# Performance work log

Hardware: AMD Instinct MI355X
Metric: run time of the kernel (lower is better)

Reference implementation:

```python
import jax, jax.numpy as jnp
import numpy as np
import math

L, D, H, PK, N = 3, 512, 8, 8, 3072
DK = D // H


def _layernorm(x, s, b):
    m = jnp.mean(x, axis=-1, keepdims=True)
    v = jnp.mean((x - m) ** 2, axis=-1, keepdims=True)
    return (x - m) / jnp.sqrt(v + 1e-6) * s + b


def setup_inputs() -> dict:
    key = jax.random.key(0)
    ks = jax.random.split(key, 12)
    p = lambda k, shape: jax.random.normal(k, shape, jnp.float32) * (1.0 / math.sqrt(shape[-1]))
    x = jax.random.normal(ks[0], (N, D), jnp.float32)
    adm = jax.random.randint(ks[1], (N, N), 0, PK, jnp.int32)
    return {
        "x": x,
        "adm": adm,
        "ln_att_s": jnp.ones((L, D), jnp.float32),
        "ln_att_b": jnp.zeros((L, D), jnp.float32),
        "Wq": p(ks[2], (L, D, D)),
        "Wk": p(ks[3], (L, D, D)),
        "Wv": p(ks[4], (L, D, D)),
        "rel_k": p(ks[5], (L, PK, DK)),
        "Wg": p(ks[6], (L, D, D)) * 0.0,  # gating weight init to 0 in original
        "bg": jnp.ones((L, D), jnp.float32),  # gating bias init to 1
        "Wo": p(ks[7], (L, D, D)),
        "bo": jnp.zeros((L, D), jnp.float32),
        "ln_ff_s": jnp.ones((L, D), jnp.float32),
        "ln_ff_b": jnp.zeros((L, D), jnp.float32),
        "W1": p(ks[8], (L, D, 2 * D)),
        "b1": jnp.zeros((L, 2 * D), jnp.float32),
        "W2": p(ks[9], (L, 2 * D, D)),
        "b2": jnp.zeros((L, D), jnp.float32),
    }


def reference(x, adm, ln_att_s, ln_att_b, Wq, Wk, Wv, rel_k, Wg, bg, Wo, bo,
              ln_ff_s, ln_ff_b, W1, b1, W2, b2):
    att_scores = []
    idx = jnp.broadcast_to(adm[None], (H, N, N))  # one_hot(gpm) @ r  ==  gather r along PK
    for n in range(L):
        xn = _layernorm(x, ln_att_s[n], ln_att_b[n])  # same layer_norm applied to x_q and x_k
        q = (xn @ Wq[n]).reshape(N, H, DK).transpose(1, 0, 2)  # [H,N,DK]
        k = (xn @ Wk[n]).reshape(N, H, DK).transpose(1, 0, 2)
        v = (xn @ Wv[n]).reshape(N, H, DK).transpose(1, 0, 2)
        attn1 = jnp.einsum('hid,hjd->hij', q, k)  # [H,N,N]
        rq = jnp.einsum('hid,pd->hip', q, rel_k[n])  # [H,N,PK]
        attn2 = jnp.take_along_axis(rq, idx, axis=2)  # [H,N,N]
        attn = jax.nn.softmax((attn1 + attn2) / math.sqrt(DK), axis=-1)
        out = jnp.einsum('hij,hjd->hid', attn, v).transpose(1, 0, 2).reshape(N, D)
        gate = jax.nn.sigmoid(xn @ Wg[n] + bg[n])
        m = (out * gate) @ Wo[n] + bo[n]
        # FFN with pre-layernorm, residual: x = x + pff(x + m)
        y = x + m
        yn = _layernorm(y, ln_ff_s[n], ln_ff_b[n])
        ff = jax.nn.gelu(yn @ W1[n] + b1[n], approximate=True) @ W2[n] + b2[n]
        x = x + ff
        att_scores.append(attn)
    return (x, jnp.stack(att_scores))
```

## Files before the change

kernel.cpp:

```cpp
#include <hip/hip_runtime.h>
#include <math.h>

#define NT 3072
#define DIM 512
#define NH 8
#define DKH 64
#define PKN 8
#define D2 1024
#define NL 3
#define QS 2048

typedef float4 f4;
typedef unsigned short ushort_t;
typedef unsigned char uchar_t;
typedef __attribute__((ext_vector_type(8))) short s8x;
typedef __attribute__((ext_vector_type(4))) float fx4;

#define MFMA(a, b, c) __builtin_amdgcn_mfma_f32_16x16x32_bf16(a, b, c, 0, 0, 0)
#define EX2(x) __builtin_amdgcn_exp2f(x)

__device__ __forceinline__ float b2f(ushort_t u) {
  union { unsigned int x; float f; } c;
  c.x = (unsigned int)u << 16;
  return c.f;
}
__device__ __forceinline__ ushort_t f2b(float f) {
  union { float f; unsigned int x; } c;
  c.f = f;
  unsigned int r = (c.x + 0x7FFFu + ((c.x >> 16) & 1u)) >> 16;
  return (ushort_t)r;
}
__device__ __forceinline__ float wred_sum(float v) {
#pragma unroll
  for (int off = 32; off > 0; off >>= 1) v += __shfl_xor(v, off);
  return v;
}
__device__ __forceinline__ void gload16(const ushort_t* g, ushort_t* l) {
  __builtin_amdgcn_global_load_lds(
      (const __attribute__((address_space(1))) unsigned int*)(const void*)g,
      (__attribute__((address_space(3))) unsigned int*)(void*)l, 16, 0, 0);
}

__global__ __launch_bounds__(256) void ln_bf16_kernel(
    const float* __restrict__ x, const float* __restrict__ s,
    const float* __restrict__ b, ushort_t* __restrict__ out) {
  int row = blockIdx.x;
  const float* xr = x + (size_t)row * DIM;
  int t = threadIdx.x;
  float v0 = xr[t], v1 = xr[t + 256];
  float sum = wred_sum(v0 + v1);
  float sq = wred_sum(v0 * v0 + v1 * v1);
  __shared__ float ss[4], s2[4];
  if ((t & 63) == 0) { ss[t >> 6] = sum; s2[t >> 6] = sq; }
  __syncthreads();
  float tot = ss[0] + ss[1] + ss[2] + ss[3];
  float tot2 = s2[0] + s2[1] + s2[2] + s2[3];
  float mean = tot * (1.0f / DIM);
  float var = tot2 * (1.0f / DIM) - mean * mean;
  float inv = rsqrtf(var + 1e-6f);
  ushort_t* orow = out + (size_t)row * DIM;
  orow[t] = f2b((v0 - mean) * inv * s[t] + b[t]);
  orow[t + 256] = f2b((v1 - mean) * inv * s[t + 256] + b[t + 256]);
}

__device__ __forceinline__ void tconv_body(const float* __restrict__ W,
                                           ushort_t* __restrict__ Wt, int K,
                                           int Nc, int tx, int ty) {
  __shared__ float Ls[64][65];
  int t = threadIdx.x;
  int n0 = tx * 64, k0 = ty * 64;
  int rr = t >> 4, cc = (t & 15) * 4;
#pragma unroll
  for (int p = 0; p < 4; ++p) {
    f4 v = *(const f4*)&W[(size_t)(k0 + rr + p * 16) * Nc + n0 + cc];
    Ls[rr + p * 16][cc + 0] = v.x;
    Ls[rr + p * 16][cc + 1] = v.y;
    Ls[rr + p * 16][cc + 2] = v.z;
    Ls[rr + p * 16][cc + 3] = v.w;
  }
  __syncthreads();
  int nr = t >> 2, kc = (t & 3) * 16;
  ushort_t tmp[16];
#pragma unroll
  for (int e = 0; e < 16; ++e) tmp[e] = f2b(Ls[kc + e][nr]);
  ushort_t* dst = &Wt[(size_t)(n0 + nr) * K + k0 + kc];
  *(uint4*)dst = *(uint4*)&tmp[0];
  *(uint4*)(dst + 8) = *(uint4*)&tmp[8];
}

__global__ __launch_bounds__(256) void wprep_kernel(
    const float* __restrict__ Wq, const float* __restrict__ Wk,
    const float* __restrict__ Wv, const float* __restrict__ Wg,
    const float* __restrict__ Wo, const float* __restrict__ W1,
    const float* __restrict__ W2, ushort_t* __restrict__ Wt) {
  int bid = blockIdx.x;
  if (bid < 320) {
    int job = bid >> 6, tile = bid & 63;
    const float* src = job == 0 ? Wq : job == 1 ? Wk : job == 2 ? Wv
                       : job == 3 ? Wg : Wo;
    tconv_body(src, Wt + (size_t)job * 262144, 512, 512, tile & 7, tile >> 3);
  } else if (bid < 448) {
    int tile = bid - 320;
    tconv_body(W1, Wt + 1310720, 512, 1024, tile & 15, tile >> 4);
  } else {
    int tile = bid - 448;
    tconv_body(W2, Wt + 1835008, 1024, 512, tile & 7, tile >> 3);
  }
}

__global__ __launch_bounds__(256) void adm8_kernel(const int* __restrict__ adm,
                                                   uchar_t* __restrict__ out) {
  size_t i = ((size_t)blockIdx.x * 256 + threadIdx.x) * 4;
  int4 v = *(const int4*)&adm[i];
  unsigned int b = (unsigned)(v.x & 255) | ((unsigned)(v.y & 255) << 8) |
                   ((unsigned)(v.z & 255) << 16) | ((unsigned)(v.w & 255) << 24);
  *(unsigned int*)&out[i] = b;
}

__global__ __launch_bounds__(256) void vt_kernel(const ushort_t* __restrict__ v,
                                                 ushort_t* __restrict__ vbT) {
  int jt = blockIdx.x, h = blockIdx.y;
  __shared__ ushort_t L[64][72];
  int t = threadIdx.x;
  int r = t >> 2, c = (t & 3) * 16;
  const ushort_t* src = v + (size_t)(jt * 64 + r) * QS + h * 64 + c;
  *(uint4*)&L[r][c] = *(const uint4*)src;
  *(uint4*)&L[r][c + 8] = *(const uint4*)(src + 8);
  __syncthreads();
  int d = t >> 2, j0 = (t & 3) * 16;
  ushort_t tmp[16];
#pragma unroll
  for (int e = 0; e < 16; ++e) tmp[e] = L[j0 + e][d];
  ushort_t* dst = vbT + (size_t)(h * 64 + d) * NT + jt * 64 + j0;
  *(uint4*)dst = *(uint4*)&tmp[0];
  *(uint4*)(dst + 8) = *(uint4*)&tmp[8];
}

template <int ACT, bool OBF>
__global__ __launch_bounds__(256) void gemm64(
    const ushort_t* __restrict__ A, const ushort_t* __restrict__ Bt,
    const float* __restrict__ bias, const float* __restrict__ res,
    void* __restrict__ Cp, int K, int ldc, float scale) {
  __shared__ __align__(16) ushort_t As[2][4096];
  __shared__ __align__(16) ushort_t Bs[2][4096];
  int t = threadIdx.x;
  int i0 = blockIdx.y * 64, j0 = blockIdx.x * 64;
  int w = t >> 6, l = t & 63;
  int wm = w >> 1, wn = w & 1;
  int lr = l >> 4, lc = l & 15;
  int sr = t >> 3;
  int sc8 = ((t & 7) ^ (sr & 7)) * 8;
  const ushort_t* aS = A + (size_t)(i0 + sr) * K + sc8;
  const ushort_t* bS = Bt + (size_t)(j0 + sr) * K + sc8;
  int sA0 = (wm * 32 + lc) * 64 + ((lr ^ (lc & 7)) * 8);
  int sA1 = (wm * 32 + 16 + lc) * 64 + ((lr ^ (lc & 7)) * 8);
  int sB0 = (wn * 32 + lc) * 64 + ((lr ^ (lc & 7)) * 8);
  int sB1 = (wn * 32 + 16 + lc) * 64 + ((lr ^ (lc & 7)) * 8);

  fx4 acc[2][2] = {};

#define G64_STAGE(buf, k0)                                                   \
  {                                                                          \
    gload16(aS + (k0), &As[buf][t * 8]);                                     \
    gload16(aS + (k0) + (size_t)32 * K, &As[buf][2048 + t * 8]);             \
    gload16(bS + (k0), &Bs[buf][t * 8]);                                     \
    gload16(bS + (k0) + (size_t)32 * K, &Bs[buf][2048 + t * 8]);             \
  }

  G64_STAGE(0, 0);
  __syncthreads();
  int cur = 0;
  for (int k0 = 0; k0 < K; k0 += 64) {
    if (k0 + 64 < K) G64_STAGE(cur ^ 1, k0 + 64);
    const ushort_t* Ac = As[cur];
    const ushort_t* Bc = Bs[cur];
#pragma unroll
    for (int ks = 0; ks < 2; ++ks) {
      s8x a0 = *(const s8x*)&Ac[sA0 ^ (ks << 5)];
      s8x a1 = *(const s8x*)&Ac[sA1 ^ (ks << 5)];
      s8x b0 = *(const s8x*)&Bc[sB0 ^ (ks << 5)];
      s8x b1 = *(const s8x*)&Bc[sB1 ^ (ks << 5)];
      acc[0][0] = MFMA(a0, b0, acc[0][0]);
      acc[0][1] = MFMA(a0, b1, acc[0][1]);
      acc[1][0] = MFMA(a1, b0, acc[1][0]);
      acc[1][1] = MFMA(a1, b1, acc[1][1]);
    }
    __syncthreads();
    cur ^= 1;
  }
#undef G64_STAGE

#pragma unroll
  for (int ms = 0; ms < 2; ++ms) {
#pragma unroll
    for (int ns = 0; ns < 2; ++ns) {
#pragma unroll
      for (int r = 0; r < 4; ++r) {
        int i = i0 + wm * 32 + ms * 16 + lr * 4 + r;
        int j = j0 + wn * 32 + ns * 16 + lc;
        float o = acc[ms][ns][r] * scale;
        if (ACT == 3) {
          if (blockIdx.x < 8) o *= 0.18033688011112042f;
          if (blockIdx.x >= 24) {
            o += bias[j & 511];
            o = 1.0f / (1.0f + __expf(-o));
          }
        } else {
          if (bias) o += bias[j];
          if (ACT == 1) {
            o = 1.0f / (1.0f + __expf(-o));
          } else if (ACT == 2) {
            float xx = o;
            float c2 = 1.5957691216057308f * (xx + 0.044715f * xx * xx * xx);
            o = xx / (1.0f + __expf(-c2));
          }
          if (res) o += res[(size_t)i * ldc + j];
        }
        if (OBF)
          ((ushort_t*)Cp)[(size_t)i * ldc + j] = f2b(o);
        else
          ((float*)Cp)[(size_t)i * ldc + j] = o;
      }
    }
  }
}

__device__ __forceinline__ float rq_sel(const unsigned int* rqt,
                                        unsigned int idx) {
  unsigned int d01 = (idx & 2) ? rqt[1] : rqt[0];
  unsigned int d23 = (idx & 2) ? rqt[3] : rqt[2];
  unsigned int dd = (idx & 4) ? d23 : d01;
  unsigned int r = (idx & 1) ? (dd & 0xffff0000u) : (dd << 16);
  return __uint_as_float(r);
}

__global__ __launch_bounds__(256) void attn_kernel(
    const ushort_t* __restrict__ xqkvg, const ushort_t* __restrict__ vbT,
    const float* __restrict__ relk, const uchar_t* __restrict__ adm8,
    float* __restrict__ att, ushort_t* __restrict__ av) {
  int f = blockIdx.y * (NT / 32) + blockIdx.x;
  int h = f & 7;
  int i0 = (f >> 3) * 32;
  int t = threadIdx.x, w = t >> 6, l = t & 63;
  int lr = l >> 4, lc = l & 15;
  int ig = w & 1, jh = w >> 1;
  int i_loc = ig * 16 + lc;
  int i = i0 + i_loc;

  __shared__ __align__(16) ushort_t Kd[2][2][4096];
  __shared__ __align__(16) ushort_t Vd[2][2][4096];
  __shared__ __align__(16) ushort_t Ps[2][2048];
  __shared__ float MLs[2][2][16][2];

  int stgo = ig * 2048;
  int srow = ig * 32 + (l >> 3);
  int kp8 = ((l & 7) ^ ((l >> 3) & 7)) * 8;
  const ushort_t* kSrc0 =
      xqkvg + 512 + (size_t)(jh * 64 + srow) * QS + h * 64 + kp8;
  const ushort_t* vSrc0 = vbT + (size_t)(h * 64 + srow) * NT + jh * 64 + kp8;
  const uchar_t* admp0 = adm8 + (size_t)i * NT + jh * 64 + lr * 4;

#define STAGE_K(buf, tt)                                                     \
  {                                                                          \
    const ushort_t* ks_ = kSrc0 + (size_t)(tt) * 128 * QS;                   \
    gload16(ks_, Kd[buf][jh] + stgo);                                        \
    gload16(ks_ + (size_t)8 * QS, Kd[buf][jh] + stgo + 512);                 \
    gload16(ks_ + (size_t)16 * QS, Kd[buf][jh] + stgo + 1024);               \
    gload16(ks_ + (size_t)24 * QS, Kd[buf][jh] + stgo + 1536);               \
  }
#define STAGE_V(buf, tt)                                                     \
  {                                                                          \
    const ushort_t* vs_ = vSrc0 + (tt) * 128;                                \
    gload16(vs_, Vd[buf][jh] + stgo);                                        \
    gload16(vs_ + (size_t)8 * NT, Vd[buf][jh] + stgo + 512);                 \
    gload16(vs_ + (size_t)16 * NT, Vd[buf][jh] + stgo + 1024);               \
    gload16(vs_ + (size_t)24 * NT, Vd[buf][jh] + stgo + 1536);               \
  }

  STAGE_K(0, 0);

  const ushort_t* qp = xqkvg + (size_t)i * QS + h * 64 + lr * 8;
  s8x qf0 = *(const s8x*)qp;
  s8x qf1 = *(const s8x*)(qp + 32);

  unsigned int rqt[4];
  {
    const ushort_t* q0 = (const ushort_t*)&qf0;
    const ushort_t* q1 = (const ushort_t*)&qf1;
    float sp[8];
#pragma unroll
    for (int p = 0; p < 8; ++p) {
      const float* rp = relk + p * 64 + lr * 8;
      float s = 0.f;
#pragma unroll
      for (int e = 0; e < 8; ++e) s = fmaf(b2f(q0[e]), rp[e], s);
#pragma unroll
      for (int e = 0; e < 8; ++e) s = fmaf(b2f(q1[e]), rp[32 + e], s);
      s += __shfl_xor(s, 16);
      s += __shfl_xor(s, 32);
      sp[p] = s;
    }
#pragma unroll
    for (int j = 0; j < 4; ++j)
      rqt[j] = (unsigned int)f2b(sp[2 * j]) |
               ((unsigned int)f2b(sp[2 * j + 1]) << 16);
  }

  int sw = (lc & 7);
  int a_b0 = lc * 64 + ((lr ^ sw) << 3);
  int a_b1 = lc * 64 + (((4 + lr) ^ sw) << 3);
  int pb0 = i_loc * 64 + ((lr ^ sw) << 3);
  int pb1 = i_loc * 64 + (((4 + lr) ^ sw) << 3);
  int swz8 = sw << 3;

  float m_run = -1e30f, l_run = 0.f;
  __syncthreads();

  {
    int cur = 0;
    for (int tt = 0; tt < 24; ++tt) {
      if (tt < 23) STAGE_K(cur ^ 1, tt + 1);
      const ushort_t* KS = Kd[cur][jh];
      const uchar_t* admp = admp0 + tt * 128;
      fx4 sacc[4] = {};
#pragma unroll
      for (int ja = 0; ja < 4; ++ja) {
        s8x a0 = *(const s8x*)(KS + a_b0 + ja * 1024);
        s8x a1 = *(const s8x*)(KS + a_b1 + ja * 1024);
        sacc[ja] = MFMA(a0, qf0, sacc[ja]);
        sacc[ja] = MFMA(a1, qf1, sacc[ja]);
      }
      float sv[4][4];
      float tm = -1e30f;
#pragma unroll
      for (int ja = 0; ja < 4; ++ja) {
        unsigned int aw = *(const unsigned int*)(admp + ja * 16);
#pragma unroll
        for (int r = 0; r < 4; ++r) {
          float vv = sacc[ja][r] + rq_sel(rqt, (aw >> (8 * r)) & 7u);
          sv[ja][r] = vv;
          tm = fmaxf(tm, vv);
        }
      }
      float mn = fmaxf(m_run, tm);
      float sum = 0.f;
#pragma unroll
      for (int ja = 0; ja < 4; ++ja)
#pragma unroll
        for (int r = 0; r < 4; ++r) sum += EX2(sv[ja][r] - mn);
      l_run = l_run * EX2(m_run - mn) + sum;
      m_run = mn;
      __syncthreads();
      cur ^= 1;
    }
  }

  STAGE_K(0, 0);
  STAGE_V(0, 0);

#pragma unroll
  for (int off = 16; off <= 32; off <<= 1) {
    float mo = __shfl_xor(m_run, off), lo = __shfl_xor(l_run, off);
    float mn = fmaxf(m_run, mo);
    l_run = l_run * EX2(m_run - mn) + lo * EX2(mo - mn);
    m_run = mn;
  }
  if (l < 16) {
    MLs[jh][ig][lc][0] = m_run;
    MLs[jh][ig][lc][1] = l_run;
  }
  __syncthreads();
  {
    float mo = MLs[jh ^ 1][ig][lc][0], lo = MLs[jh ^ 1][ig][lc][1];
    float mn = fmaxf(m_run, mo);
    l_run = l_run * EX2(m_run - mn) + lo * EX2(mo - mn);
    m_run = mn;
  }
  float lofs = m_run + __log2f(l_run);

  fx4 oacc[4] = {};
  float* attb = att + ((size_t)h * NT + i0) * NT;
  ushort_t* PS = Ps[jh];
  int jh64 = jh * 64;
  {
    int cur = 0;
    for (int tt = 0; tt < 24; ++tt) {
      if (tt < 23) {
        STAGE_K(cur ^ 1, tt + 1);
        STAGE_V(cur ^ 1, tt + 1);
      }
      const ushort_t* KS = Kd[cur][jh];
      const ushort_t* VS = Vd[cur][jh];
      const uchar_t* admp = admp0 + tt * 128;
      fx4 sacc[4] = {};
#pragma unroll
      for (int ja = 0; ja < 4; ++ja) {
        s8x a0 = *(const s8x*)(KS + a_b0 + ja * 1024);
        s8x a1 = *(const s8x*)(KS + a_b1 + ja * 1024);
        sacc[ja] = MFMA(a0, qf0, sacc[ja]);
        sacc[ja] = MFMA(a1, qf1, sacc[ja]);
      }
#pragma unroll
      for (int ja = 0; ja < 4; ++ja) {
        unsigned int aw = *(const unsigned int*)(admp + ja * 16);
        float p0 = EX2(sacc[ja][0] + rq_sel(rqt, aw & 7u) - lofs);
        float p1 = EX2(sacc[ja][1] + rq_sel(rqt, (aw >> 8) & 7u) - lofs);
        float p2 = EX2(sacc[ja][2] + rq_sel(rqt, (aw >> 16) & 7u) - lofs);
        float p3 = EX2(sacc[ja][3] + rq_sel(rqt, (aw >> 24) & 7u) - lofs);
        unsigned int w01 = (unsigned int)f2b(p0) | ((unsigned int)f2b(p1) << 16);
        unsigned int w23 = (unsigned int)f2b(p2) | ((unsigned int)f2b(p3) << 16);
        int cb = ja * 16 + lr * 4;
        *(unsigned int*)&PS[i_loc * 64 + (cb ^ swz8)] = w01;
        *(unsigned int*)&PS[i_loc * 64 + ((cb + 2) ^ swz8)] = w23;
      }
      {
        int uu = ig * 64 + l;
        int row = uu >> 2, cs = (uu & 3) * 16;
        int rsw = (row & 7) << 3;
        uint4 A_ = *(const uint4*)&PS[row * 64 + (cs ^ rsw)];
        uint4 B_ = *(const uint4*)&PS[row * 64 + ((cs + 8) ^ rsw)];
        const ushort_t* ap = (const ushort_t*)&A_;
        const ushort_t* bp = (const ushort_t*)&B_;
        float* op = attb + (size_t)row * NT + tt * 128 + jh64 + cs;
        f4 o0 = {b2f(ap[0]), b2f(ap[1]), b2f(ap[2]), b2f(ap[3])};
        f4 o1 = {b2f(ap[4]), b2f(ap[5]), b2f(ap[6]), b2f(ap[7])};
        f4 o2 = {b2f(bp[0]), b2f(bp[1]), b2f(bp[2]), b2f(bp[3])};
        f4 o3 = {b2f(bp[4]), b2f(bp[5]), b2f(bp[6]), b2f(bp[7])};
        *(f4*)(op + 0) = o0;
        *(f4*)(op + 4) = o1;
        *(f4*)(op + 8) = o2;
        *(f4*)(op + 12) = o3;
      }
#pragma unroll
      for (int ks = 0; ks < 2; ++ks) {
        s8x pf = *(const s8x*)(PS + (ks == 0 ? pb0 : pb1));
#pragma unroll
        for (int nd = 0; nd < 4; ++nd) {
          s8x vf = *(const s8x*)(VS + (ks == 0 ? a_b0 : a_b1) + nd * 1024);
          oacc[nd] = MFMA(vf, pf, oacc[nd]);
        }
      }
      __syncthreads();
      cur ^= 1;
    }
  }
#undef STAGE_K
#undef STAGE_V

  ushort_t* PsF = &Ps[0][0];
  int swzO = (i_loc & 7) << 3;
  if (jh == 1) {
#pragma unroll
    for (int nd = 0; nd < 4; ++nd) {
      int d0 = nd * 16 + lr * 4;
      unsigned int lo = (unsigned int)f2b(oacc[nd][0]) |
                        ((unsigned int)f2b(oacc[nd][1]) << 16);
      unsigned int hi = (unsigned int)f2b(oacc[nd][2]) |
                        ((unsigned int)f2b(oacc[nd][3]) << 16);
      uint2 pk = {lo, hi};
      *(uint2*)&PsF[i_loc * 64 + (d0 ^ swzO)] = pk;
    }
  }
  __syncthreads();
  if (jh == 0) {
    const ushort_t* gp = xqkvg + (size_t)i * QS + 1536 + h * 64;
#pragma unroll
    for (int nd = 0; nd < 4; ++nd) {
      int d0 = nd * 16 + lr * 4;
      uint2 pk = *(const uint2*)&PsF[i_loc * 64 + (d0 ^ swzO)];
      const ushort_t* pp = (const ushort_t*)&pk;
      uint2 gk = *(const uint2*)(gp + d0);
      const ushort_t* gg = (const ushort_t*)&gk;
      ushort_t ot[4];
#pragma unroll
      for (int r = 0; r < 4; ++r)
        ot[r] = f2b((oacc[nd][r] + b2f(pp[r])) * b2f(gg[r]));
      *(uint2*)&av[(size_t)i * DIM + h * 64 + d0] = *(uint2*)ot;
    }
  }
}

extern "C" void kernel_launch(void* const* d_in, const int* in_sizes, int n_in,
                              void* d_out, int out_size, void* d_ws,
                              size_t ws_size, hipStream_t stream) {
  const float* x_in = (const float*)d_in[0];
  const int* adm = (const int*)d_in[1];
  const float* ln_att_s = (const float*)d_in[2];
  const float* ln_att_b = (const float*)d_in[3];
  const float* Wq = (const float*)d_in[4];
  const float* Wk = (const float*)d_in[5];
  const float* Wv = (const float*)d_in[6];
  const float* rel_k = (const float*)d_in[7];
  const float* Wg = (const float*)d_in[8];
  const float* bg = (const float*)d_in[9];
  const float* Wo = (const float*)d_in[10];
  const float* bo = (const float*)d_in[11];
  const float* ln_ff_s = (const float*)d_in[12];
  const float* ln_ff_b = (const float*)d_in[13];
  const float* W1 = (const float*)d_in[14];
  const float* b1 = (const float*)d_in[15];
  const float* W2 = (const float*)d_in[16];
  const float* b2 = (const float*)d_in[17];
  float* out = (float*)d_out;

  const size_t ND = (size_t)NT * DIM;
  char* ws = (char*)d_ws;
  float* x_cur = (float*)ws;
  float* y = (float*)(ws + 6291456);
  ushort_t* xqkvg = (ushort_t*)(ws + 12582912);
  ushort_t* avb = (ushort_t*)(ws + 25165824);
  ushort_t* xnb = (ushort_t*)(ws + 28311552);
  ushort_t* vbT = (ushort_t*)(ws + 31457280);
  uchar_t* adm8 = (uchar_t*)(ws + 34603008);
  ushort_t* Wt = (ushort_t*)(ws + 44040192);
  ushort_t* h1b = xqkvg;

  hipMemcpyAsync(x_cur, x_in, ND * sizeof(float), hipMemcpyDeviceToDevice,
                 stream);
  adm8_kernel<<<(NT * NT) / 1024, 256, 0, stream>>>(adm, adm8);

  dim3 gQKVG(32, NT / 64);
  dim3 gA(8, NT / 64);
  dim3 gF1(16, NT / 64);

  for (int n = 0; n < NL; ++n) {
    float* att = out + ND + (size_t)n * NH * NT * NT;
    size_t wo = (size_t)n * DIM * DIM;

    wprep_kernel<<<576, 256, 0, stream>>>(Wq + wo, Wk + wo, Wv + wo, Wg + wo,
                                          Wo + wo, W1 + (size_t)n * DIM * D2,
                                          W2 + (size_t)n * D2 * DIM, Wt);
    ln_bf16_kernel<<<NT, 256, 0, stream>>>(x_cur, ln_att_s + n * DIM,
                                           ln_att_b + n * DIM, xnb);
    gemm64<3, true><<<gQKVG, 256, 0, stream>>>(xnb, Wt, bg + n * DIM, nullptr,
                                               xqkvg, DIM, QS, 1.0f);
    vt_kernel<<<dim3(NT / 64, NH), 256, 0, stream>>>(xqkvg + 1024, vbT);
    attn_kernel<<<dim3(NT / 32, NH), 256, 0, stream>>>(
        xqkvg, vbT, rel_k + n * PKN * DKH, adm8, att, avb);
    gemm64<0, false><<<gA, 256, 0, stream>>>(avb, Wt + 1048576, bo + n * DIM,
                                             x_cur, y, DIM, DIM, 1.0f);
    ln_bf16_kernel<<<NT, 256, 0, stream>>>(y, ln_ff_s + n * DIM,
                                           ln_ff_b + n * DIM, xnb);
    gemm64<2, true><<<gF1, 256, 0, stream>>>(xnb, Wt + 1310720, b1 + n * D2,
                                             nullptr, h1b, DIM, D2, 1.0f);
    gemm64<0, false><<<gA, 256, 0, stream>>>(h1b, Wt + 1835008, b2 + n * DIM,
                                             x_cur, x_cur, D2, DIM, 1.0f);
  }
  hipMemcpyAsync(out, x_cur, ND * sizeof(float), hipMemcpyDeviceToDevice,
                 stream);
}
```

Before: 1.057 ms.

## Batch weight prep, drop residual copies, use nontemporal attention stores

Weight transpose/convert for all three layers now runs in one launch indexed by blockIdx.y, instead of one launch per layer. The initial and final device-to-device copies of x are removed: layer 0 reads x_in directly and the last FFN GEMM writes straight into the output. Attention-probability writes to the large score tensor become nontemporal stores, which keeps them from polluting cache. A __syncthreads is inserted before the P tile is read back from shared memory, which looks like a race fix but adds one barrier per iteration.

```diff
diff --git a/kernel.cpp b/kernel.cpp
--- a/kernel.cpp
+++ b/kernel.cpp
@@ -93,18 +93,23 @@
     const float* __restrict__ Wv, const float* __restrict__ Wg,
     const float* __restrict__ Wo, const float* __restrict__ W1,
     const float* __restrict__ W2, ushort_t* __restrict__ Wt) {
+  int n = blockIdx.y;
+  size_t wo5 = (size_t)n * 262144;
+  ushort_t* Wtl = Wt + (size_t)n * 2359296;
   int bid = blockIdx.x;
   if (bid < 320) {
     int job = bid >> 6, tile = bid & 63;
-    const float* src = job == 0 ? Wq : job == 1 ? Wk : job == 2 ? Wv
-                       : job == 3 ? Wg : Wo;
-    tconv_body(src, Wt + (size_t)job * 262144, 512, 512, tile & 7, tile >> 3);
+    const float* src = job == 0 ? Wq + wo5 : job == 1 ? Wk + wo5
+                       : job == 2 ? Wv + wo5 : job == 3 ? Wg + wo5 : Wo + wo5;
+    tconv_body(src, Wtl + (size_t)job * 262144, 512, 512, tile & 7, tile >> 3);
   } else if (bid < 448) {
     int tile = bid - 320;
-    tconv_body(W1, Wt + 1310720, 512, 1024, tile & 15, tile >> 4);
+    tconv_body(W1 + (size_t)n * 524288, Wtl + 1310720, 512, 1024, tile & 15,
+               tile >> 4);
   } else {
     int tile = bid - 448;
-    tconv_body(W2, Wt + 1835008, 1024, 512, tile & 7, tile >> 3);
+    tconv_body(W2 + (size_t)n * 524288, Wtl + 1835008, 1024, 512, tile & 7,
+               tile >> 3);
   }
 }
 
@@ -413,6 +418,7 @@
         *(unsigned int*)&PS[i_loc * 64 + (cb ^ swz8)] = w01;
         *(unsigned int*)&PS[i_loc * 64 + ((cb + 2) ^ swz8)] = w23;
       }
+      __syncthreads();
       {
         int uu = ig * 64 + l;
         int row = uu >> 2, cs = (uu & 3) * 16;
@@ -422,14 +428,14 @@
         const ushort_t* ap = (const ushort_t*)&A_;
         const ushort_t* bp = (const ushort_t*)&B_;
         float* op = attb + (size_t)row * NT + tt * 128 + jh64 + cs;
-        f4 o0 = {b2f(ap[0]), b2f(ap[1]), b2f(ap[2]), b2f(ap[3])};
-        f4 o1 = {b2f(ap[4]), b2f(ap[5]), b2f(ap[6]), b2f(ap[7])};
-        f4 o2 = {b2f(bp[0]), b2f(bp[1]), b2f(bp[2]), b2f(bp[3])};
-        f4 o3 = {b2f(bp[4]), b2f(bp[5]), b2f(bp[6]), b2f(bp[7])};
-        *(f4*)(op + 0) = o0;
-        *(f4*)(op + 4) = o1;
-        *(f4*)(op + 8) = o2;
-        *(f4*)(op + 12) = o3;
+        fx4 o0 = {b2f(ap[0]), b2f(ap[1]), b2f(ap[2]), b2f(ap[3])};
+        fx4 o1 = {b2f(ap[4]), b2f(ap[5]), b2f(ap[6]), b2f(ap[7])};
+        fx4 o2 = {b2f(bp[0]), b2f(bp[1]), b2f(bp[2]), b2f(bp[3])};
+        fx4 o3 = {b2f(bp[4]), b2f(bp[5]), b2f(bp[6]), b2f(bp[7])};
+        __builtin_nontemporal_store(o0, (fx4*)(op + 0));
+        __builtin_nontemporal_store(o1, (fx4*)(op + 4));
+        __builtin_nontemporal_store(o2, (fx4*)(op + 8));
+        __builtin_nontemporal_store(o3, (fx4*)(op + 12));
       }
 #pragma unroll
       for (int ks = 0; ks < 2; ++ks) {
@@ -515,9 +521,9 @@
   ushort_t* Wt = (ushort_t*)(ws + 44040192);
   ushort_t* h1b = xqkvg;
 
-  hipMemcpyAsync(x_cur, x_in, ND * sizeof(float), hipMemcpyDeviceToDevice,
-                 stream);
   adm8_kernel<<<(NT * NT) / 1024, 256, 0, stream>>>(adm, adm8);
+  wprep_kernel<<<dim3(576, 3), 256, 0, stream>>>(Wq, Wk, Wv, Wg, Wo, W1, W2,
+                                                 Wt);
 
   dim3 gQKVG(32, NT / 64);
   dim3 gA(8, NT / 64);
@@ -525,27 +531,24 @@
 
   for (int n = 0; n < NL; ++n) {
     float* att = out + ND + (size_t)n * NH * NT * NT;
-    size_t wo = (size_t)n * DIM * DIM;
-
-    wprep_kernel<<<576, 256, 0, stream>>>(Wq + wo, Wk + wo, Wv + wo, Wg + wo,
-                                          Wo + wo, W1 + (size_t)n * DIM * D2,
-                                          W2 + (size_t)n * D2 * DIM, Wt);
-    ln_bf16_kernel<<<NT, 256, 0, stream>>>(x_cur, ln_att_s + n * DIM,
+    const float* xprev = (n == 0) ? x_in : x_cur;
+    float* xout = (n == NL - 1) ? out : x_cur;
+    ushort_t* Wtl = Wt + (size_t)n * 2359296;
+
+    ln_bf16_kernel<<<NT, 256, 0, stream>>>(xprev, ln_att_s + n * DIM,
                                            ln_att_b + n * DIM, xnb);
-    gemm64<3, true><<<gQKVG, 256, 0, stream>>>(xnb, Wt, bg + n * DIM, nullptr,
+    gemm64<3, true><<<gQKVG, 256, 0, stream>>>(xnb, Wtl, bg + n * DIM, nullptr,
                                                xqkvg, DIM, QS, 1.0f);
     vt_kernel<<<dim3(NT / 64, NH), 256, 0, stream>>>(xqkvg + 1024, vbT);
     attn_kernel<<<dim3(NT / 32, NH), 256, 0, stream>>>(
         xqkvg, vbT, rel_k + n * PKN * DKH, adm8, att, avb);
-    gemm64<0, false><<<gA, 256, 0, stream>>>(avb, Wt + 1048576, bo + n * DIM,
-                                             x_cur, y, DIM, DIM, 1.0f);
+    gemm64<0, false><<<gA, 256, 0, stream>>>(avb, Wtl + 1048576, bo + n * DIM,
+                                             xprev, y, DIM, DIM, 1.0f);
     ln_bf16_kernel<<<NT, 256, 0, stream>>>(y, ln_ff_s + n * DIM,
                                            ln_ff_b + n * DIM, xnb);
-    gemm64<2, true><<<gF1, 256, 0, stream>>>(xnb, Wt + 1310720, b1 + n * D2,
+    gemm64<2, true><<<gF1, 256, 0, stream>>>(xnb, Wtl + 1310720, b1 + n * D2,
                                              nullptr, h1b, DIM, D2, 1.0f);
-    gemm64<0, false><<<gA, 256, 0, stream>>>(h1b, Wt + 1835008, b2 + n * DIM,
-                                             x_cur, x_cur, D2, DIM, 1.0f);
-  }
-  hipMemcpyAsync(out, x_cur, ND * sizeof(float), hipMemcpyDeviceToDevice,
-                 stream);
-}
+    gemm64<0, false><<<gA, 256, 0, stream>>>(h1b, Wtl + 1835008, b2 + n * DIM,
+                                             xprev, xout, D2, DIM, 1.0f);
+  }
+}
```

After: 1.421 ms. +34.4%, slower.
